# Performance work log

Hardware: AMD Instinct MI355X
Metric: run time of the kernel (lower is better)

The kernel has to match this reference:

```python
import jax, jax.numpy as jnp
import numpy as np

N = 262144        # 64^3 grid unknowns
NNZ = 7 * N       # ~7-point stencil sparsity
BS = 32


def setup_inputs() -> dict:
    key = jax.random.key(0)
    k1, k2, k3, k4, k5 = jax.random.split(key, 5)
    y_pred = jax.random.normal(k1, (BS, N), dtype=jnp.float32)
    y_true = jax.random.normal(k2, (BS, N), dtype=jnp.float32)
    A_vals = jax.random.normal(k3, (NNZ,), dtype=jnp.float32)
    A_rows = jax.random.randint(k4, (NNZ,), 0, N, dtype=jnp.int32)
    A_cols = jax.random.randint(k5, (NNZ,), 0, N, dtype=jnp.int32)
    return {"y_pred": y_pred, "y_true": y_true, "A_vals": A_vals,
            "A_rows": A_rows, "A_cols": A_cols}


def reference(y_pred, y_true, A_vals, A_rows, A_cols):
    # YhatY[b] = <y_true[b], y_pred[b]>
    YhatY = jnp.sum(y_true * y_pred, axis=1)                      # (bs,)
    # Sparse matvec per batch: YhatAt = (A @ y_pred.T).T, COO form.
    # gathered[e, b] = A_vals[e] * y_pred[b, A_cols[e]]
    gathered = (y_pred[:, A_cols] * A_vals).T                     # (nnz, bs)
    YhatAt = jax.ops.segment_sum(gathered, A_rows, num_segments=N).T  # (bs, N)
    # YhatYhatAt[b] = <y_pred[b], A y_pred[b]>
    YhatYhatAt = jnp.sum(y_pred * YhatAt, axis=1)                 # (bs,)
    # diag(YhatY / YhatYhatAt) @ YhatAt == row-wise scale by alpha
    alpha = YhatY / YhatYhatAt                                    # (bs,)
    resid = y_true - alpha[:, None] * YhatAt                      # (bs, N)
    return jnp.mean(jnp.sum(resid * resid, axis=1))
```

## Files before the change

### kernel.cpp

```cpp
#include <hip/hip_runtime.h>

#define NGRID 262144
#define NNZ_C 1835008
#define TP    260
#define NS    256
#define TPAD  260

#define FPSCALE   524288.0f
#define FPINV     (1.0f / 524288.0f)


__global__ __launch_bounds__(256) void k_prep(
        const float* __restrict__ yp, float* __restrict__ yp_t,
        float* __restrict__ yat_t) {
    __shared__ __align__(16) float T[32 * TP];
    const int tid = threadIdx.x;
    const int l = tid & 63, w = tid >> 6;
    const size_t n0 = (size_t)blockIdx.x * 256;
    #pragma unroll
    for (int s = 0; s < 8; ++s) {
        const int b = s * 4 + w;
        const float4 a = *(const float4*)(yp + (size_t)b * NGRID + n0 + 4 * l);
        *(float4*)(&T[b * TP + 4 * l]) = a;
    }
    __syncthreads();
    float4* dst4 = (float4*)(yp_t + n0 * 32);
    float4* yat4 = (float4*)(yat_t + n0 * 32);
    #pragma unroll
    for (int q = 0; q < 8; ++q) {
        const int f = q * 256 + tid;
        const int n = f >> 3;
        const int bb = 4 * (f & 7);
        float4 v;
        v.x = T[(bb + 0) * TP + n];
        v.y = T[(bb + 1) * TP + n];
        v.z = T[(bb + 2) * TP + n];
        v.w = T[(bb + 3) * TP + n];
        dst4[f] = v;
        yat4[f] = make_float4(0.f, 0.f, 0.f, 0.f);
    }
}

__global__ void k_scatter(const float* __restrict__ vals,
                          const int* __restrict__ rows,
                          const int* __restrict__ cols,
                          const float* __restrict__ yp_t,
                          unsigned long long* __restrict__ yat64) {
    const size_t tid = (size_t)blockIdx.x * blockDim.x + threadIdx.x;
    const int b2 = (int)(tid & 15);
    const size_t e = tid >> 4;
    const float v = vals[e];
    const int r = rows[e];
    const int c = cols[e];
    const float2 x2 = *(const float2*)(yp_t + (size_t)c * 32 + 2 * b2);
    const long long i0 = (long long)__float2int_rn(v * x2.x * FPSCALE);
    const long long i1 = (long long)__float2int_rn(v * x2.y * FPSCALE);
    const unsigned long long pk = (unsigned long long)((i1 << 32) + i0);
    atomicAdd(&yat64[(size_t)r * 16 + b2], pk);
}

__global__ __launch_bounds__(256) void k_post(
        const unsigned long long* __restrict__ yat64,
        const float* __restrict__ yp, const float* __restrict__ yt,
        float* __restrict__ p2) {
    __shared__ __align__(16) float T[32 * TPAD];
    const int tid = threadIdx.x;
    const int g = blockIdx.x;
    const size_t n0 = (size_t)g * NS;
    const ulonglong2* y2 = (const ulonglong2*)(yat64 + n0 * 16);
    #pragma unroll
    for (int q = 0; q < 8; ++q) {
        const int f = q * 256 + tid;
        const int n = f >> 3;
        const int b0 = 4 * (f & 7);
        const ulonglong2 pv = y2[f];
        const int lo0 = (int)(unsigned)pv.x;
        const int hi0 = (int)((pv.x + 0x80000000ULL) >> 32);
        const int lo1 = (int)(unsigned)pv.y;
        const int hi1 = (int)((pv.y + 0x80000000ULL) >> 32);
        T[(b0 + 0) * TPAD + n] = (float)lo0 * FPINV;
        T[(b0 + 1) * TPAD + n] = (float)hi0 * FPINV;
        T[(b0 + 2) * TPAD + n] = (float)lo1 * FPINV;
        T[(b0 + 3) * TPAD + n] = (float)hi1 * FPINV;
    }
    __syncthreads();
    const int b = tid >> 3, j = tid & 7;
    const float* ytb = yt + (size_t)b * NGRID + n0;
    const float* ypb = yp + (size_t)b * NGRID + n0;
    const float* Tb = &T[b * TPAD];
    float c1 = 0.f, c2 = 0.f, c3 = 0.f, st = 0.f, sy = 0.f;
    #pragma unroll
    for (int s = 0; s < NS / 32; ++s) {
        const int n = 4 * j + 32 * s;
        const float4 a = *(const float4*)(Tb + n);
        const float4 t = *(const float4*)(ytb + n);
        const float4 p = *(const float4*)(ypb + n);
        c1 = fmaf(p.x, a.x, c1); c2 = fmaf(t.x, a.x, c2);
        c3 = fmaf(a.x, a.x, c3); st = fmaf(t.x, t.x, st);
        sy = fmaf(t.x, p.x, sy);
        c1 = fmaf(p.y, a.y, c1); c2 = fmaf(t.y, a.y, c2);
        c3 = fmaf(a.y, a.y, c3); st = fmaf(t.y, t.y, st);
        sy = fmaf(t.y, p.y, sy);
        c1 = fmaf(p.z, a.z, c1); c2 = fmaf(t.z, a.z, c2);
        c3 = fmaf(a.z, a.z, c3); st = fmaf(t.z, t.z, st);
        sy = fmaf(t.z, p.z, sy);
        c1 = fmaf(p.w, a.w, c1); c2 = fmaf(t.w, a.w, c2);
        c3 = fmaf(a.w, a.w, c3); st = fmaf(t.w, t.w, st);
        sy = fmaf(t.w, p.w, sy);
    }
    #pragma unroll
    for (int d = 4; d; d >>= 1) {
        c1 += __shfl_down(c1, d, 8);
        c2 += __shfl_down(c2, d, 8);
        c3 += __shfl_down(c3, d, 8);
        st += __shfl_down(st, d, 8);
        sy += __shfl_down(sy, d, 8);
    }
    if (j == 0) {
        float* row = p2 + (size_t)g * 160;
        row[0 * 32 + b] = c1;
        row[1 * 32 + b] = c2;
        row[2 * 32 + b] = c3;
        row[3 * 32 + b] = st;
        row[4 * 32 + b] = sy;
    }
}

__global__ __launch_bounds__(256) void k_finish1(
        const float* __restrict__ p2, float* __restrict__ pr2) {
    const int tid = threadIdx.x, g = blockIdx.x;
    if (tid < 160) {
        float acc = 0.f;
        #pragma unroll
        for (int j = 0; j < 32; ++j) acc += p2[(size_t)(g * 32 + j) * 160 + tid];
        pr2[g * 160 + tid] = acc;
    }
}

__global__ __launch_bounds__(256) void k_finish2(
        const float* __restrict__ pr2, float* __restrict__ out) {
    __shared__ float tot[160];
    __shared__ float lb[32];
    const int tid = threadIdx.x;
    if (tid < 160) {
        float acc = 0.f;
        #pragma unroll
        for (int j = 0; j < 32; ++j) acc += pr2[j * 160 + tid];
        tot[tid] = acc;
    }
    __syncthreads();
    if (tid < 32) {
        const float c1 = tot[0 + tid];
        const float c2 = tot[32 + tid];
        const float c3 = tot[64 + tid];
        const float stt = tot[96 + tid];
        const float sty = tot[128 + tid];
        const float a = sty / c1;
        lb[tid] = fmaf(a * a, c3, fmaf(-2.f * a, c2, stt));
    }
    __syncthreads();
    if (tid == 0) {
        float s = 0.f;
        #pragma unroll
        for (int i = 0; i < 32; ++i) s += lb[i];
        out[0] = s * (1.0f / 32.0f);
    }
}

extern "C" void kernel_launch(void* const* d_in, const int* in_sizes, int n_in,
                              void* d_out, int out_size, void* d_ws, size_t ws_size,
                              hipStream_t stream) {
    const float* yp = (const float*)d_in[0];
    const float* yt = (const float*)d_in[1];
    const float* Av = (const float*)d_in[2];
    const int*   Ar = (const int*)d_in[3];
    const int*   Ac = (const int*)d_in[4];
    float* out = (float*)d_out;

    float* ws    = (float*)d_ws;
    float* yp_t  = ws;
    float* yat_f = yp_t + (size_t)NGRID * 32;
    unsigned long long* yat64 = (unsigned long long*)yat_f;
    float* p2    = yat_f + (size_t)NGRID * 32;
    float* pr2   = p2 + 1024 * 160;

    k_prep<<<1024, 256, 0, stream>>>(yp, yp_t, yat_f);
    k_scatter<<<(NNZ_C * 16) / 256, 256, 0, stream>>>(Av, Ar, Ac, yp_t, yat64);
    k_post<<<1024, 256, 0, stream>>>(yat64, yp, yt, p2);
    k_finish1<<<32, 256, 0, stream>>>(p2, pr2);
    k_finish2<<<1, 256, 0, stream>>>(pr2, out);
}
```

Baseline: 298.4 us.

## Use persistent-grid scatter, halve post tile, and replace tree reduction with atomics

The scatter kernel now runs a fixed 2048-block grid in which each thread loops over strided edge chunks, replacing the one-thread-per-edge-pair launch. The post kernel processes 128 grid points per block and accumulates its partial sums directly into a zeroed 160-float buffer with float atomics. This removes the two finish-reduction kernels and their intermediate buffers. In exchange, float atomic accumulation makes the summation order nondeterministic, and the 160 addresses may see atomic contention.

```diff
diff --git a/kernel.cpp b/kernel.cpp
--- a/kernel.cpp
+++ b/kernel.cpp
@@ -3,8 +3,8 @@
 #define NGRID 262144
 #define NNZ_C 1835008
 #define TP    260
-#define NS    256
-#define TPAD  260
+#define NS    128
+#define TPAD  132
 
 #define FPSCALE   524288.0f
 #define FPINV     (1.0f / 524288.0f)
@@ -12,9 +12,10 @@
 
 __global__ __launch_bounds__(256) void k_prep(
         const float* __restrict__ yp, float* __restrict__ yp_t,
-        float* __restrict__ yat_t) {
+        float* __restrict__ yat_t, float* __restrict__ tot) {
     __shared__ __align__(16) float T[32 * TP];
     const int tid = threadIdx.x;
+    if (blockIdx.x == 0 && tid < 160) tot[tid] = 0.f;
     const int l = tid & 63, w = tid >> 6;
     const size_t n0 = (size_t)blockIdx.x * 256;
     #pragma unroll
@@ -41,35 +42,38 @@
     }
 }
 
-__global__ void k_scatter(const float* __restrict__ vals,
-                          const int* __restrict__ rows,
-                          const int* __restrict__ cols,
-                          const float* __restrict__ yp_t,
-                          unsigned long long* __restrict__ yat64) {
-    const size_t tid = (size_t)blockIdx.x * blockDim.x + threadIdx.x;
-    const int b2 = (int)(tid & 15);
-    const size_t e = tid >> 4;
-    const float v = vals[e];
-    const int r = rows[e];
-    const int c = cols[e];
-    const float2 x2 = *(const float2*)(yp_t + (size_t)c * 32 + 2 * b2);
-    const long long i0 = (long long)__float2int_rn(v * x2.x * FPSCALE);
-    const long long i1 = (long long)__float2int_rn(v * x2.y * FPSCALE);
-    const unsigned long long pk = (unsigned long long)((i1 << 32) + i0);
-    atomicAdd(&yat64[(size_t)r * 16 + b2], pk);
+__global__ __launch_bounds__(256) void k_scatter(
+        const float* __restrict__ vals, const int* __restrict__ rows,
+        const int* __restrict__ cols, const float* __restrict__ yp_t,
+        unsigned long long* __restrict__ yat64) {
+    const int tid = threadIdx.x;
+    const int b2 = tid & 15;
+    const size_t g0 = ((size_t)blockIdx.x * 256 + tid) >> 4;
+    #pragma unroll 2
+    for (int it = 0; it < NNZ_C / 32768; ++it) {
+        const size_t e = g0 + (size_t)it * 32768;
+        const float v = vals[e];
+        const int r = rows[e];
+        const int c = cols[e];
+        const float2 x2 = *(const float2*)(yp_t + (size_t)c * 32 + 2 * b2);
+        const long long i0 = (long long)__float2int_rn(v * x2.x * FPSCALE);
+        const long long i1 = (long long)__float2int_rn(v * x2.y * FPSCALE);
+        atomicAdd(&yat64[(size_t)r * 16 + b2],
+                  (unsigned long long)((i1 << 32) + i0));
+    }
 }
 
 __global__ __launch_bounds__(256) void k_post(
         const unsigned long long* __restrict__ yat64,
         const float* __restrict__ yp, const float* __restrict__ yt,
-        float* __restrict__ p2) {
+        float* __restrict__ tot) {
     __shared__ __align__(16) float T[32 * TPAD];
     const int tid = threadIdx.x;
     const int g = blockIdx.x;
     const size_t n0 = (size_t)g * NS;
     const ulonglong2* y2 = (const ulonglong2*)(yat64 + n0 * 16);
     #pragma unroll
-    for (int q = 0; q < 8; ++q) {
+    for (int q = 0; q < 4; ++q) {
         const int f = q * 256 + tid;
         const int n = f >> 3;
         const int b0 = 4 * (f & 7);
@@ -117,38 +121,18 @@
         sy += __shfl_down(sy, d, 8);
     }
     if (j == 0) {
-        float* row = p2 + (size_t)g * 160;
-        row[0 * 32 + b] = c1;
-        row[1 * 32 + b] = c2;
-        row[2 * 32 + b] = c3;
-        row[3 * 32 + b] = st;
-        row[4 * 32 + b] = sy;
+        atomicAdd(&tot[0 * 32 + b], c1);
+        atomicAdd(&tot[1 * 32 + b], c2);
+        atomicAdd(&tot[2 * 32 + b], c3);
+        atomicAdd(&tot[3 * 32 + b], st);
+        atomicAdd(&tot[4 * 32 + b], sy);
     }
 }
 
-__global__ __launch_bounds__(256) void k_finish1(
-        const float* __restrict__ p2, float* __restrict__ pr2) {
-    const int tid = threadIdx.x, g = blockIdx.x;
-    if (tid < 160) {
-        float acc = 0.f;
-        #pragma unroll
-        for (int j = 0; j < 32; ++j) acc += p2[(size_t)(g * 32 + j) * 160 + tid];
-        pr2[g * 160 + tid] = acc;
-    }
-}
-
-__global__ __launch_bounds__(256) void k_finish2(
-        const float* __restrict__ pr2, float* __restrict__ out) {
-    __shared__ float tot[160];
+__global__ __launch_bounds__(64) void k_finish(
+        const float* __restrict__ tot, float* __restrict__ out) {
     __shared__ float lb[32];
     const int tid = threadIdx.x;
-    if (tid < 160) {
-        float acc = 0.f;
-        #pragma unroll
-        for (int j = 0; j < 32; ++j) acc += pr2[j * 160 + tid];
-        tot[tid] = acc;
-    }
-    __syncthreads();
     if (tid < 32) {
         const float c1 = tot[0 + tid];
         const float c2 = tot[32 + tid];
@@ -181,12 +165,10 @@
     float* yp_t  = ws;
     float* yat_f = yp_t + (size_t)NGRID * 32;
     unsigned long long* yat64 = (unsigned long long*)yat_f;
-    float* p2    = yat_f + (size_t)NGRID * 32;
-    float* pr2   = p2 + 1024 * 160;
+    float* tot   = yat_f + (size_t)NGRID * 32;
 
-    k_prep<<<1024, 256, 0, stream>>>(yp, yp_t, yat_f);
-    k_scatter<<<(NNZ_C * 16) / 256, 256, 0, stream>>>(Av, Ar, Ac, yp_t, yat64);
-    k_post<<<1024, 256, 0, stream>>>(yat64, yp, yt, p2);
-    k_finish1<<<32, 256, 0, stream>>>(p2, pr2);
-    k_finish2<<<1, 256, 0, stream>>>(pr2, out);
+    k_prep<<<1024, 256, 0, stream>>>(yp, yp_t, yat_f, tot);
+    k_scatter<<<2048, 256, 0, stream>>>(Av, Ar, Ac, yp_t, yat64);
+    k_post<<<2048, 256, 0, stream>>>(yat64, yp, yt, tot);
+    k_finish<<<1, 64, 0, stream>>>(tot, out);
 }
```

Result: slower. 382.9 us (+28.3%).
